# Performance work log

Hardware: AMD Instinct MI355X
Metric: run time of the kernel (lower is better)

Reference implementation:

```python
import jax, jax.numpy as jnp
import numpy as np

B, S, D = 1, 2048, 2048
H = 16
Q_LORA = 1536
KV_LORA = 512
NOPE = 128
ROPE = 64
VD = 128
QHD = NOPE + ROPE  # 192
THETA = 50000.0
EPS = 1e-6


def rmsnorm(x, w, eps=EPS):
    xf = x.astype(jnp.float32)
    var = jnp.mean(xf * xf, axis=-1, keepdims=True)
    return (w * (xf * jax.lax.rsqrt(var + eps)).astype(x.dtype))


def rotate_half(x):
    x1, x2 = jnp.split(x, 2, axis=-1)
    return jnp.concatenate([-x2, x1], axis=-1)


def deinterleave(x):
    # view(..., d//2, 2).transpose(-1,-2).reshape(..., d): [x0,x2,...,x1,x3,...]
    b, h, s, d = x.shape
    return x.reshape(b, h, s, d // 2, 2).swapaxes(-1, -2).reshape(b, h, s, d)


def setup_inputs() -> dict:
    key = jax.random.key(0)
    ks = jax.random.split(key, 8)
    sc = 0.02
    return {
        "hidden_states": jax.random.normal(ks[0], (B, S, D), jnp.float32),
        "position_ids": jnp.broadcast_to(jnp.arange(S, dtype=jnp.int32), (B, S)),
        "q_a_w": jax.random.normal(ks[1], (Q_LORA, D), jnp.float32) * sc,
        "q_a_ln_w": jnp.ones((Q_LORA,), jnp.float32),
        "q_b_w": jax.random.normal(ks[2], (H * QHD, Q_LORA), jnp.float32) * sc,
        "kv_a_w": jax.random.normal(ks[3], (KV_LORA + ROPE, D), jnp.float32) * sc,
        "kv_a_ln_w": jnp.ones((KV_LORA,), jnp.float32),
        "kv_b_w": jax.random.normal(ks[4], (H * (NOPE + VD), KV_LORA), jnp.float32) * sc,
        "o_w": jax.random.normal(ks[5], (D, H * VD), jnp.float32) * sc,
    }


def reference(hidden_states, position_ids, q_a_w, q_a_ln_w, q_b_w, kv_a_w, kv_a_ln_w, kv_b_w, o_w):
    bsz, q_len, _ = hidden_states.shape
    # low-rank Q: q_b(rmsnorm(q_a(x)))
    q = rmsnorm(hidden_states @ q_a_w.T, q_a_ln_w) @ q_b_w.T
    q = q.reshape(bsz, q_len, H, QHD).transpose(0, 2, 1, 3)  # [b,h,s,192]
    q_nope, q_pe = q[..., :NOPE], q[..., NOPE:]
    # compressed KV + shared rope key
    ckv = hidden_states @ kv_a_w.T  # [b,s,512+64]
    compressed_kv, k_pe = ckv[..., :KV_LORA], ckv[..., KV_LORA:]
    k_pe = k_pe.reshape(bsz, q_len, 1, ROPE).transpose(0, 2, 1, 3)  # [b,1,s,64]
    kv = rmsnorm(compressed_kv, kv_a_ln_w) @ kv_b_w.T
    kv = kv.reshape(bsz, q_len, H, NOPE + VD).transpose(0, 2, 1, 3)
    k_nope, value_states = kv[..., :NOPE], kv[..., NOPE:]
    # rotary cache
    inv_freq = 1.0 / (THETA ** (jnp.arange(0, ROPE, 2, dtype=jnp.float32) / ROPE))
    t = jnp.arange(q_len, dtype=jnp.float32)
    freqs = jnp.outer(t, inv_freq)
    emb = jnp.concatenate([freqs, freqs], axis=-1)  # [s,64]
    cos = jnp.cos(emb)[position_ids][:, None]  # [b,1,s,64]
    sin = jnp.sin(emb)[position_ids][:, None]
    q_pe = deinterleave(q_pe)
    k_pe = deinterleave(k_pe)
    q_pe = q_pe * cos + rotate_half(q_pe) * sin
    k_pe = k_pe * cos + rotate_half(k_pe) * sin
    query_states = jnp.concatenate([q_nope, q_pe], axis=-1)  # [b,h,s,192]
    key_states = jnp.concatenate([k_nope, jnp.broadcast_to(k_pe, (bsz, H, q_len, ROPE))], axis=-1)
    scale = QHD ** (-0.5)
    scores = jnp.einsum('bhqd,bhkd->bhqk', query_states, key_states) * scale
    causal = jnp.tril(jnp.ones((q_len, q_len), bool))
    scores = jnp.where(causal, scores, jnp.finfo(scores.dtype).min)
    attn = jax.nn.softmax(scores, axis=-1)
    out = jnp.einsum('bhqk,bhkd->bhqd', attn, value_states)  # [b,h,s,128]
    out = out.transpose(0, 2, 1, 3).reshape(bsz, q_len, H * VD)
    return out @ o_w.T
```

## Files before the change

### kernel.cpp

```cpp
#include <hip/hip_runtime.h>
#include <hip/hip_bf16.h>
#include <cmath>

#define S_LEN 2048
#define D_MODEL 2048
#define N_HEADS 16
#define Q_LORA 1536
#define KV_LORA 512
#define NOPE 128
#define ROPE_D 64
#define VD 128
#define QHD 192
#define AC_W 2112

typedef __attribute__((ext_vector_type(8))) short bf16x8;
typedef __attribute__((ext_vector_type(4))) float f32x4;
typedef __attribute__((ext_vector_type(16))) float f32x16;
typedef __attribute__((ext_vector_type(4))) unsigned short u16x4;

static __device__ __forceinline__ unsigned short f2u(float x) {
  union { float f; unsigned u; } v; v.f = x;
  unsigned r = v.u + 0x7fffu + ((v.u >> 16) & 1u);
  return (unsigned short)(r >> 16);
}
static __device__ __forceinline__ unsigned short f2u_fast(float x) {
  union { float f; unsigned u; } v; v.f = x;
  return (unsigned short)((v.u + 0x8000u) >> 16);
}
static __device__ __forceinline__ float u2f(unsigned short x) {
  union { unsigned u; float f; } v; v.u = ((unsigned)x) << 16;
  return v.f;
}

#define AS1 __attribute__((address_space(1)))
#define AS3 __attribute__((address_space(3)))
static __device__ __forceinline__ void gload_lds16(const unsigned short* g, unsigned short* l) {
  __builtin_amdgcn_global_load_lds((const AS1 unsigned int*)g, (AS3 unsigned int*)l, 16, 0, 0);
}

__global__ __launch_bounds__(256) void conv_bf16(const float* __restrict__ src,
                                                 unsigned short* __restrict__ dst,
                                                 int n4, float scale) {
  for (int i = blockIdx.x * 256 + threadIdx.x; i < n4; i += gridDim.x * 256) {
    const float4 v = ((const float4*)src)[i];
    u16x4 o;
    o[0] = f2u(v.x * scale); o[1] = f2u(v.y * scale);
    o[2] = f2u(v.z * scale); o[3] = f2u(v.w * scale);
    ((u16x4*)dst)[i] = o;
  }
}

__global__ __launch_bounds__(256) void conv2_bf16(const float* __restrict__ srcA, int n4a,
                                                  const float* __restrict__ srcB, int n4total,
                                                  unsigned short* __restrict__ dst) {
  for (int i = blockIdx.x * 256 + threadIdx.x; i < n4total; i += gridDim.x * 256) {
    const float4 v = (i < n4a) ? ((const float4*)srcA)[i] : ((const float4*)srcB)[i - n4a];
    u16x4 o;
    o[0] = f2u(v.x); o[1] = f2u(v.y); o[2] = f2u(v.z); o[3] = f2u(v.w);
    ((u16x4*)dst)[i] = o;
  }
}

template <int MODE>
__global__ __launch_bounds__(256) void gemm_mfma(const unsigned short* __restrict__ A,
                                                 const unsigned short* __restrict__ W,
                                                 void* __restrict__ Cv,
                                                 unsigned short* __restrict__ C2,
                                                 int N, int K) {
  __shared__ unsigned short As[2][8192];
  __shared__ unsigned short Ws[2][4096];
  const int tid = threadIdx.x;
  const int wave = tid >> 6, lane = tid & 63;
  const int col16 = lane & 15, g = lane >> 4;
  const int arow = blockIdx.y * 128, wrow = blockIdx.x * 64;
  const int wm = (wave >> 1) * 64, wn = (wave & 1) * 32;

  const unsigned short* gA[4];
  const unsigned short* gW[2];
  int dA[4], dW[2];
#pragma unroll
  for (int i = 0; i < 4; ++i) {
    const int c = i * 256 + tid;
    const int r = c >> 3, sl = c & 7;
    gA[i] = A + (size_t)(arow + r) * K + (sl ^ (r & 7)) * 8;
    dA[i] = c * 8;
  }
#pragma unroll
  for (int i = 0; i < 2; ++i) {
    const int c = i * 256 + tid;
    const int r = c >> 3, sl = c & 7;
    gW[i] = W + (size_t)(wrow + r) * K + (sl ^ (r & 7)) * 8;
    dW[i] = c * 8;
  }

  f32x4 acc[4][2];
#pragma unroll
  for (int i = 0; i < 4; ++i)
#pragma unroll
    for (int j = 0; j < 2; ++j) acc[i][j] = (f32x4){0.f, 0.f, 0.f, 0.f};

#pragma unroll
  for (int i = 0; i < 4; ++i) gload_lds16(gA[i], &As[0][dA[i]]);
#pragma unroll
  for (int i = 0; i < 2; ++i) gload_lds16(gW[i], &Ws[0][dW[i]]);

  int cur = 0;
  for (int k0 = 0; k0 < K; k0 += 64) {
    __syncthreads();
    if (k0 + 64 < K) {
      const int b = cur ^ 1, kk = k0 + 64;
#pragma unroll
      for (int i = 0; i < 4; ++i) gload_lds16(gA[i] + kk, &As[b][dA[i]]);
#pragma unroll
      for (int i = 0; i < 2; ++i) gload_lds16(gW[i] + kk, &Ws[b][dW[i]]);
    }
#pragma unroll
    for (int kh = 0; kh < 2; ++kh) {
      bf16x8 af[4], bfr[2];
#pragma unroll
      for (int i = 0; i < 4; ++i) {
        const int row = wm + i * 16 + col16;
        af[i] = *(const bf16x8*)(&As[cur][row * 64 + (((kh * 4 + g) ^ (row & 7)) * 8)]);
      }
#pragma unroll
      for (int j = 0; j < 2; ++j) {
        const int row = wn + j * 16 + col16;
        bfr[j] = *(const bf16x8*)(&Ws[cur][row * 64 + (((kh * 4 + g) ^ (row & 7)) * 8)]);
      }
#pragma unroll
      for (int i = 0; i < 4; ++i)
#pragma unroll
        for (int j = 0; j < 2; ++j)
          acc[i][j] = __builtin_amdgcn_mfma_f32_16x16x32_bf16(af[i], bfr[j], acc[i][j], 0, 0, 0);
    }
    cur ^= 1;
  }

#pragma unroll
  for (int i = 0; i < 4; ++i)
#pragma unroll
    for (int j = 0; j < 2; ++j) {
      const int col = wrow + wn + j * 16 + col16;
      const int row0 = arow + wm + i * 16 + g * 4;
#pragma unroll
      for (int r = 0; r < 4; ++r) {
        if constexpr (MODE == 0)
          ((float*)Cv)[(size_t)(row0 + r) * N + col] = acc[i][j][r];
        else if constexpr (MODE == 1)
          ((unsigned short*)Cv)[(size_t)(row0 + r) * N + col] = f2u(acc[i][j][r]);
        else {
          const int hh = col >> 8, d = col & 255;
          if (d < NOPE)
            C2[((size_t)hh * S_LEN + row0 + r) * QHD + d] = f2u(acc[i][j][r]);
          else
            ((unsigned short*)Cv)[(size_t)(row0 + r) * (N_HEADS * 256) + col] = f2u(acc[i][j][r]);
        }
      }
    }
}

__global__ __launch_bounds__(256) void rmsnorm_kernel(const float* __restrict__ src, int src_ld,
                                                      const float* __restrict__ w,
                                                      unsigned short* __restrict__ dst, int dst_ld,
                                                      int dim) {
  const int row = blockIdx.x;
  const float* x = src + (size_t)row * src_ld;
  float ss = 0.f;
  for (int i = threadIdx.x; i < dim; i += 256) {
    float v = x[i];
    ss += v * v;
  }
#pragma unroll
  for (int off = 32; off; off >>= 1) ss += __shfl_xor(ss, off);
  __shared__ float red[4];
  const int wv = threadIdx.x >> 6, ln = threadIdx.x & 63;
  if (ln == 0) red[wv] = ss;
  __syncthreads();
  const float tot = red[0] + red[1] + red[2] + red[3];
  const float scale = rsqrtf(tot / (float)dim + 1e-6f);
  for (int i = threadIdx.x; i < dim; i += 256) {
    dst[(size_t)row * dst_ld + i] = f2u(w[i] * (x[i] * scale));
  }
}

__global__ void rope_kernel(unsigned short* __restrict__ q, const float* __restrict__ ac,
                            unsigned short* __restrict__ Kb, const int* __restrict__ pos_ids) {
  const int s = blockIdx.x;
  const int j = threadIdx.x;
  const float t = (float)pos_ids[s];
  const float invf = powf(50000.0f, -(float)(2 * j) / 64.0f);
  const float ang = t * invf;
  const float c = cosf(ang), sn = sinf(ang);
  for (int h = 0; h < N_HEADS; ++h) {
    unsigned short* base = q + (size_t)s * (N_HEADS * QHD) + h * QHD + NOPE;
    const float x0 = u2f(base[2 * j]), x1 = u2f(base[2 * j + 1]);
    __syncthreads();
    base[j] = f2u(x0 * c - x1 * sn);
    base[32 + j] = f2u(x1 * c + x0 * sn);
    __syncthreads();
  }
  const float* kb = ac + (size_t)s * AC_W + 2048;
  const unsigned short r0 = f2u(kb[2 * j] * c - kb[2 * j + 1] * sn);
  const unsigned short r1 = f2u(kb[2 * j + 1] * c + kb[2 * j] * sn);
#pragma unroll
  for (int h = 0; h < N_HEADS; ++h) {
    unsigned short* kd = Kb + ((size_t)h * S_LEN + s) * QHD + NOPE;
    kd[j] = r0;
    kd[32 + j] = r1;
  }
}

__global__ __launch_bounds__(256) void build_vt(const unsigned short* __restrict__ kv,
                                                unsigned short* __restrict__ Vt) {
  __shared__ unsigned short t[32][33];
  const int s0 = blockIdx.x * 32, d0 = blockIdx.y * 32, h = blockIdx.z;
  const int tx = threadIdx.x & 31, ty = threadIdx.x >> 5;
#pragma unroll
  for (int i = 0; i < 4; ++i) {
    const int s = s0 + ty + i * 8;
    t[ty + i * 8][tx] = kv[(size_t)s * (N_HEADS * 256) + h * 256 + NOPE + d0 + tx];
  }
  __syncthreads();
  const int g16 = tx >> 4, k16 = tx & 15;
  const int h2 = (k16 >> 2) & 1;
  const int jj = (k16 & 3) + 4 * ((k16 >> 3) & 1);
  const int p = g16 * 16 + h2 * 8 + jj;
#pragma unroll
  for (int i = 0; i < 4; ++i) {
    const int d = d0 + ty + i * 8;
    Vt[((size_t)h * VD + d) * S_LEN + s0 + p] = t[tx][ty + i * 8];
  }
}

__global__ __launch_bounds__(256) void flash_attn(const unsigned short* __restrict__ Q,
                                                  const unsigned short* __restrict__ Kb,
                                                  const unsigned short* __restrict__ Vt,
                                                  unsigned short* __restrict__ Pb,
                                                  float2* __restrict__ mlb) {
  __shared__ unsigned short Ks[2][32 * QHD];
  __shared__ unsigned short Vs[2][VD * 32];
  const int tid = threadIdx.x;
  const int wave = tid >> 6, lane = tid & 63;
  const int q5 = lane & 31, h2 = lane >> 5;
  const int lin = (int)blockIdx.x;
  const int h = ((lin & 7) << 1) | ((lin >> 3) & 1);
  const int s = (lin >> 4) & 3;
  const int z = lin >> 6;
  const int za = z >> 2, zb = z & 3;
  const int t = 4 * za + ((za + zb) & 3);
  const int qw = t * 128 + wave * 32;
  const int qr = qw + q5;

  bf16x8 qf[12];
  {
    const unsigned short* qrow = Q + (size_t)qr * (N_HEADS * QHD) + h * QHD + h2 * 8;
#pragma unroll
    for (int i = 0; i < 12; ++i) qf[i] = *(const bf16x8*)(qrow + i * 16);
  }

  const unsigned short* KbH = Kb + (size_t)h * S_LEN * QHD;
  const unsigned short* VtH = Vt + (size_t)h * VD * S_LEN;

  int eK[3], eV[2];
#pragma unroll
  for (int i = 0; i < 3; ++i) {
    const int c = i * 256 + tid;
    const int r = c / 24, sl = c - r * 24;
    eK[i] = r * QHD + (((sl & 24) | ((sl & 7) ^ (r & 7)))) * 8;
  }
#pragma unroll
  for (int i = 0; i < 2; ++i) {
    const int c = i * 256 + tid;
    const int d = c >> 2, sl = c & 3;
    eV[i] = d * S_LEN + ((sl ^ (d & 3))) * 8;
  }

  int xK[12];
#pragma unroll
  for (int i = 0; i < 12; ++i) {
    const int sg = 2 * i + h2;
    xK[i] = q5 * QHD + (((sg & 24) | ((sg & 7) ^ (q5 & 7)))) * 8;
  }
  int xV[2];
#pragma unroll
  for (int i = 0; i < 2; ++i) xV[i] = q5 * 32 + (((i * 2 + h2) ^ (q5 & 3))) * 8;

  f32x16 o[4];
#pragma unroll
  for (int i = 0; i < 4; ++i)
#pragma unroll
    for (int r = 0; r < 16; ++r) o[i][r] = 0.f;
  float m = -1e30f, l = 0.f;

  const int nT = t + 1;

  {
    const unsigned short* kp = KbH + (size_t)s * 32 * QHD;
    const unsigned short* vp = VtH + s * 32;
#pragma unroll
    for (int i = 0; i < 3; ++i) gload_lds16(kp + eK[i], &Ks[0][(i * 256 + tid) * 8]);
#pragma unroll
    for (int i = 0; i < 2; ++i) gload_lds16(vp + eV[i], &Vs[0][(i * 256 + tid) * 8]);
  }

  for (int it = 0; it < nT; ++it) {
    __syncthreads();
    if (it + 1 < nT) {
      const int jn = 4 * (it + 1) + s;
      const unsigned short* kp = KbH + (size_t)jn * 32 * QHD;
      const unsigned short* vp = VtH + jn * 32;
      const int b = (it + 1) & 1;
#pragma unroll
      for (int i = 0; i < 3; ++i) gload_lds16(kp + eK[i], &Ks[b][(i * 256 + tid) * 8]);
#pragma unroll
      for (int i = 0; i < 2; ++i) gload_lds16(vp + eV[i], &Vs[b][(i * 256 + tid) * 8]);
    }
    const int k0 = 32 * (4 * it + s);
    if (k0 <= qw + 31) {
      const unsigned short* Ksc = Ks[it & 1];
      const unsigned short* Vsc = Vs[it & 1];

      f32x16 c;
#pragma unroll
      for (int r = 0; r < 16; ++r) c[r] = 0.f;
      __builtin_amdgcn_s_setprio(1);
#pragma unroll
      for (int dt = 0; dt < 12; ++dt) {
        const bf16x8 a = *(const bf16x8*)(Ksc + xK[dt]);
        c = __builtin_amdgcn_mfma_f32_32x32x16_bf16(a, qf[dt], c, 0, 0, 0);
      }
      __builtin_amdgcn_s_setprio(0);

      if (k0 + 31 > qw) {
#pragma unroll
        for (int r = 0; r < 16; ++r) {
          const int kk = k0 + (r & 3) + 8 * (r >> 2) + 4 * h2;
          if (kk > qr) c[r] = -1e30f;
        }
      }
      float bm = c[0];
#pragma unroll
      for (int r = 1; r < 16; ++r) bm = fmaxf(bm, c[r]);
      bm = fmaxf(bm, __shfl_xor(bm, 32));
      const bool skip = __all(bm <= m + 8.f);
      const float mn = skip ? m : fmaxf(m, bm);
      float ps = 0.f;
      bf16x8 pb0, pb1;
#pragma unroll
      for (int r = 0; r < 8; ++r) {
        const float p0 = exp2f(c[r] - mn);
        const float p1 = exp2f(c[8 + r] - mn);
        ps += p0 + p1;
        pb0[r] = (short)f2u_fast(p0);
        pb1[r] = (short)f2u_fast(p1);
      }
      ps += __shfl_xor(ps, 32);
      if (skip) {
        l += ps;
      } else {
        const float corr = exp2f(m - mn);
        l = l * corr + ps;
        m = mn;
#pragma unroll
        for (int i = 0; i < 4; ++i)
#pragma unroll
          for (int r = 0; r < 16; ++r) o[i][r] *= corr;
      }
      __builtin_amdgcn_s_setprio(1);
#pragma unroll
      for (int db = 0; db < 4; ++db) {
        const bf16x8 va0 = *(const bf16x8*)(Vsc + db * 1024 + xV[0]);
        o[db] = __builtin_amdgcn_mfma_f32_32x32x16_bf16(va0, pb0, o[db], 0, 0, 0);
        const bf16x8 va1 = *(const bf16x8*)(Vsc + db * 1024 + xV[1]);
        o[db] = __builtin_amdgcn_mfma_f32_32x32x16_bf16(va1, pb1, o[db], 0, 0, 0);
      }
      __builtin_amdgcn_s_setprio(0);
    }
  }

  unsigned short* pr = Pb + (((size_t)qr * 4 + s) * N_HEADS + h) * VD;
#pragma unroll
  for (int db = 0; db < 4; ++db)
#pragma unroll
    for (int rq = 0; rq < 4; ++rq) {
      const int d0 = db * 32 + 4 * h2 + 8 * rq;
      u16x4 w4;
      w4[0] = f2u(o[db][rq * 4 + 0]);
      w4[1] = f2u(o[db][rq * 4 + 1]);
      w4[2] = f2u(o[db][rq * 4 + 2]);
      w4[3] = f2u(o[db][rq * 4 + 3]);
      *(uint2*)(pr + d0) = __builtin_bit_cast(uint2, w4);
    }
  if (h2 == 0) mlb[((size_t)qr * 4 + s) * N_HEADS + h] = make_float2(m, l);
}

__global__ __launch_bounds__(256) void combine4(const unsigned short* __restrict__ Pb,
                                                const float2* __restrict__ mlb,
                                                unsigned short* __restrict__ outb) {
  const int idx = blockIdx.x * 256 + threadIdx.x;
  const int d8 = idx & 15, hq = idx >> 4;
  const int h = hq & 15, q = hq >> 4;
  float2 ml[4];
  float M = -1e30f;
#pragma unroll
  for (int s = 0; s < 4; ++s) {
    ml[s] = mlb[((size_t)q * 4 + s) * N_HEADS + h];
    M = fmaxf(M, ml[s].x);
  }
  float w[4], den = 0.f;
#pragma unroll
  for (int s = 0; s < 4; ++s) {
    w[s] = exp2f(ml[s].x - M);
    den += w[s] * ml[s].y;
  }
  const float inv = 1.f / den;
  float acc[8] = {};
#pragma unroll
  for (int s = 0; s < 4; ++s) {
    const bf16x8 v = *(const bf16x8*)(Pb + (((size_t)q * 4 + s) * N_HEADS + h) * VD + d8 * 8);
    const float ws = w[s] * inv;
#pragma unroll
    for (int e = 0; e < 8; ++e) acc[e] += u2f((unsigned short)v[e]) * ws;
  }
  u16x4 o0, o1;
#pragma unroll
  for (int e = 0; e < 4; ++e) { o0[e] = f2u(acc[e]); o1[e] = f2u(acc[4 + e]); }
  unsigned short* dst = outb + ((size_t)q * N_HEADS + h) * VD + d8 * 8;
  *(uint2*)(dst) = __builtin_bit_cast(uint2, o0);
  *(uint2*)(dst + 4) = __builtin_bit_cast(uint2, o1);
}

extern "C" void kernel_launch(void* const* d_in, const int* in_sizes, int n_in,
                              void* d_out, int out_size, void* d_ws, size_t ws_size,
                              hipStream_t stream) {
  const float* hidden    = (const float*)d_in[0];
  const int*   pos       = (const int*)d_in[1];
  const float* q_a_w     = (const float*)d_in[2];
  const float* q_a_ln_w  = (const float*)d_in[3];
  const float* q_b_w     = (const float*)d_in[4];
  const float* kv_a_w    = (const float*)d_in[5];
  const float* kv_a_ln_w = (const float*)d_in[6];
  const float* kv_b_w    = (const float*)d_in[7];
  const float* o_w       = (const float*)d_in[8];
  float* out = (float*)d_out;
  (void)in_sizes; (void)n_in; (void)out_size; (void)ws_size;

  char* base = (char*)d_ws;
  unsigned short* qbuf  = (unsigned short*)(base);
  unsigned short* kvbuf = (unsigned short*)(base + 12582912);
  unsigned short* Pbuf  = (unsigned short*)(base + 12582912);
  float2*         mlb   = (float2*)(base + 46137344);
  float*          ac    = (float*)(base + 29360128);
  unsigned short* qan   = (unsigned short*)(base + 46661632);
  unsigned short* ckvn  = (unsigned short*)(base + 52953088);
  unsigned short* Hb    = (unsigned short*)(base + 55050240);
  unsigned short* Vt    = (unsigned short*)(base + 55050240);
  unsigned short* wbuf  = (unsigned short*)(base + 63438848);
  unsigned short* attnb = (unsigned short*)(base + 72876032);
  unsigned short* Kb    = (unsigned short*)(base + 81264640);

  const dim3 b256(256);
  const float qscale = 0.07216878364870323f * 1.4426950408889634f;

  conv_bf16<<<2048, b256, 0, stream>>>(hidden, Hb, (S_LEN * D_MODEL) / 4, 1.f);

  conv2_bf16<<<2048, b256, 0, stream>>>(q_a_w, (Q_LORA * D_MODEL) / 4,
                                        kv_a_w, (AC_W * D_MODEL) / 4, wbuf);
  gemm_mfma<0><<<dim3(AC_W / 64, S_LEN / 128), b256, 0, stream>>>(Hb, wbuf, ac, nullptr, AC_W, D_MODEL);

  rmsnorm_kernel<<<S_LEN, b256, 0, stream>>>(ac, AC_W, q_a_ln_w, qan, Q_LORA, Q_LORA);
  rmsnorm_kernel<<<S_LEN, b256, 0, stream>>>(ac + Q_LORA, AC_W, kv_a_ln_w, ckvn, KV_LORA, KV_LORA);

  conv_bf16<<<2048, b256, 0, stream>>>(q_b_w, wbuf, (N_HEADS * QHD * Q_LORA) / 4, qscale);
  gemm_mfma<1><<<dim3(N_HEADS * QHD / 64, S_LEN / 128), b256, 0, stream>>>(qan, wbuf, qbuf, nullptr, N_HEADS * QHD, Q_LORA);

  conv_bf16<<<2048, b256, 0, stream>>>(kv_b_w, wbuf, (N_HEADS * 256 * KV_LORA) / 4, 1.f);
  gemm_mfma<2><<<dim3(N_HEADS * 256 / 64, S_LEN / 128), b256, 0, stream>>>(ckvn, wbuf, kvbuf, Kb, N_HEADS * 256, KV_LORA);

  rope_kernel<<<S_LEN, 32, 0, stream>>>(qbuf, ac, Kb, pos);

  build_vt<<<dim3(S_LEN / 32, VD / 32, N_HEADS), b256, 0, stream>>>(kvbuf, Vt);

  flash_attn<<<dim3(1024), b256, 0, stream>>>(qbuf, Kb, Vt, Pbuf, mlb);
  combine4<<<2048, b256, 0, stream>>>(Pbuf, mlb, attnb);

  conv_bf16<<<2048, b256, 0, stream>>>(o_w, wbuf, (D_MODEL * N_HEADS * VD) / 4, 1.f);
  gemm_mfma<0><<<dim3(D_MODEL / 64, S_LEN / 128), b256, 0, stream>>>(attnb, wbuf, out, nullptr, D_MODEL, N_HEADS * VD);
}
```

Before: 213.4 us.

## Switch flash attention from 32x32x16 to 16x16x32 MFMA tiles

Each wave now handles its 32 query rows as two 16-row halves and uses 16x16x32 bf16 MFMA instructions for both QK^T and PV. The K and V shared-memory read swizzles are redone to match, and build_vt's permutation of V columns is changed so its layout fits the new B-operand layout. The aim is better MFMA throughput or issue efficiency and a softmax that works on smaller accumulator tiles. The cost is twice the softmax bookkeeping (two running max/sum states), extra cross-lane shuffles, and more MFMA instructions per tile.

```diff
diff --git a/kernel.cpp b/kernel.cpp
--- a/kernel.cpp
+++ b/kernel.cpp
@@ -15,7 +15,6 @@
 
 typedef __attribute__((ext_vector_type(8))) short bf16x8;
 typedef __attribute__((ext_vector_type(4))) float f32x4;
-typedef __attribute__((ext_vector_type(16))) float f32x16;
 typedef __attribute__((ext_vector_type(4))) unsigned short u16x4;
 
 static __device__ __forceinline__ unsigned short f2u(float x) {
@@ -221,10 +220,7 @@
     t[ty + i * 8][tx] = kv[(size_t)s * (N_HEADS * 256) + h * 256 + NOPE + d0 + tx];
   }
   __syncthreads();
-  const int g16 = tx >> 4, k16 = tx & 15;
-  const int h2 = (k16 >> 2) & 1;
-  const int jj = (k16 & 3) + 4 * ((k16 >> 3) & 1);
-  const int p = g16 * 16 + h2 * 8 + jj;
+  const int p = ((tx & 15) >> 2) * 8 + ((tx >> 4) & 1) * 4 + (tx & 3);
 #pragma unroll
   for (int i = 0; i < 4; ++i) {
     const int d = d0 + ty + i * 8;
@@ -241,21 +237,25 @@
   __shared__ unsigned short Vs[2][VD * 32];
   const int tid = threadIdx.x;
   const int wave = tid >> 6, lane = tid & 63;
-  const int q5 = lane & 31, h2 = lane >> 5;
+  const int g = lane >> 4, col = lane & 15;
   const int lin = (int)blockIdx.x;
   const int h = ((lin & 7) << 1) | ((lin >> 3) & 1);
   const int s = (lin >> 4) & 3;
   const int z = lin >> 6;
-  const int za = z >> 2, zb = z & 3;
-  const int t = 4 * za + ((za + zb) & 3);
-  const int qw = t * 128 + wave * 32;
-  const int qr = qw + q5;
-
-  bf16x8 qf[12];
+  const int zj = z >> 2, za = z & 3;
+  const int t = 4 * zj + ((zj + za) & 3);
+  const int qwv = t * 128 + wave * 32;
+  const int qrA = qwv + col, qrB = qwv + 16 + col;
+
+  bf16x8 qfA[6], qfB[6];
   {
-    const unsigned short* qrow = Q + (size_t)qr * (N_HEADS * QHD) + h * QHD + h2 * 8;
-#pragma unroll
-    for (int i = 0; i < 12; ++i) qf[i] = *(const bf16x8*)(qrow + i * 16);
+    const unsigned short* qa = Q + (size_t)qrA * (N_HEADS * QHD) + h * QHD + g * 8;
+    const unsigned short* qb = Q + (size_t)qrB * (N_HEADS * QHD) + h * QHD + g * 8;
+#pragma unroll
+    for (int i = 0; i < 6; ++i) {
+      qfA[i] = *(const bf16x8*)(qa + i * 32);
+      qfB[i] = *(const bf16x8*)(qb + i * 32);
+    }
   }
 
   const unsigned short* KbH = Kb + (size_t)h * S_LEN * QHD;
@@ -275,22 +275,13 @@
     eV[i] = d * S_LEN + ((sl ^ (d & 3))) * 8;
   }
 
-  int xK[12];
-#pragma unroll
-  for (int i = 0; i < 12; ++i) {
-    const int sg = 2 * i + h2;
-    xK[i] = q5 * QHD + (((sg & 24) | ((sg & 7) ^ (q5 & 7)))) * 8;
-  }
-  int xV[2];
-#pragma unroll
-  for (int i = 0; i < 2; ++i) xV[i] = q5 * 32 + (((i * 2 + h2) ^ (q5 & 3))) * 8;
-
-  f32x16 o[4];
-#pragma unroll
-  for (int i = 0; i < 4; ++i)
-#pragma unroll
-    for (int r = 0; r < 16; ++r) o[i][r] = 0.f;
-  float m = -1e30f, l = 0.f;
+  f32x4 oA[8], oB[8];
+#pragma unroll
+  for (int i = 0; i < 8; ++i) {
+    oA[i] = (f32x4){0.f, 0.f, 0.f, 0.f};
+    oB[i] = (f32x4){0.f, 0.f, 0.f, 0.f};
+  }
+  float mA = -1e30f, lA = 0.f, mB = -1e30f, lB = 0.f;
 
   const int nT = t + 1;
 
@@ -302,6 +293,13 @@
 #pragma unroll
     for (int i = 0; i < 2; ++i) gload_lds16(vp + eV[i], &Vs[0][(i * 256 + tid) * 8]);
   }
+
+  int xK[6];
+#pragma unroll
+  for (int i = 0; i < 6; ++i) xK[i] = ((4 * i + g) ^ (col & 7)) * 8;
+  const int rbK = col * QHD;
+  const int xV = (g ^ (col & 3)) * 8;
+  const int rbV = col * 32;
 
   for (int it = 0; it < nT; ++it) {
     __syncthreads();
@@ -316,82 +314,122 @@
       for (int i = 0; i < 2; ++i) gload_lds16(vp + eV[i], &Vs[b][(i * 256 + tid) * 8]);
     }
     const int k0 = 32 * (4 * it + s);
-    if (k0 <= qw + 31) {
+    if (k0 <= qwv + 31) {
       const unsigned short* Ksc = Ks[it & 1];
       const unsigned short* Vsc = Vs[it & 1];
 
-      f32x16 c;
-#pragma unroll
-      for (int r = 0; r < 16; ++r) c[r] = 0.f;
+      f32x4 cA0 = (f32x4){0.f, 0.f, 0.f, 0.f}, cA1 = cA0, cB0 = cA0, cB1 = cA0;
       __builtin_amdgcn_s_setprio(1);
 #pragma unroll
-      for (int dt = 0; dt < 12; ++dt) {
-        const bf16x8 a = *(const bf16x8*)(Ksc + xK[dt]);
-        c = __builtin_amdgcn_mfma_f32_32x32x16_bf16(a, qf[dt], c, 0, 0, 0);
+      for (int dt = 0; dt < 6; ++dt) {
+        const bf16x8 a0 = *(const bf16x8*)(Ksc + rbK + xK[dt]);
+        const bf16x8 a1 = *(const bf16x8*)(Ksc + rbK + 16 * QHD + xK[dt]);
+        cA0 = __builtin_amdgcn_mfma_f32_16x16x32_bf16(a0, qfA[dt], cA0, 0, 0, 0);
+        cA1 = __builtin_amdgcn_mfma_f32_16x16x32_bf16(a1, qfA[dt], cA1, 0, 0, 0);
+        cB0 = __builtin_amdgcn_mfma_f32_16x16x32_bf16(a0, qfB[dt], cB0, 0, 0, 0);
+        cB1 = __builtin_amdgcn_mfma_f32_16x16x32_bf16(a1, qfB[dt], cB1, 0, 0, 0);
       }
       __builtin_amdgcn_s_setprio(0);
 
-      if (k0 + 31 > qw) {
-#pragma unroll
-        for (int r = 0; r < 16; ++r) {
-          const int kk = k0 + (r & 3) + 8 * (r >> 2) + 4 * h2;
-          if (kk > qr) c[r] = -1e30f;
+      if (k0 + 31 > qwv) {
+#pragma unroll
+        for (int r = 0; r < 4; ++r) {
+          const int kk = k0 + 4 * g + r;
+          if (kk > qrA) cA0[r] = -1e30f;
+          if (kk + 16 > qrA) cA1[r] = -1e30f;
+          if (kk > qrB) cB0[r] = -1e30f;
+          if (kk + 16 > qrB) cB1[r] = -1e30f;
         }
       }
-      float bm = c[0];
-#pragma unroll
-      for (int r = 1; r < 16; ++r) bm = fmaxf(bm, c[r]);
-      bm = fmaxf(bm, __shfl_xor(bm, 32));
-      const bool skip = __all(bm <= m + 8.f);
-      const float mn = skip ? m : fmaxf(m, bm);
-      float ps = 0.f;
-      bf16x8 pb0, pb1;
-#pragma unroll
-      for (int r = 0; r < 8; ++r) {
-        const float p0 = exp2f(c[r] - mn);
-        const float p1 = exp2f(c[8 + r] - mn);
-        ps += p0 + p1;
-        pb0[r] = (short)f2u_fast(p0);
-        pb1[r] = (short)f2u_fast(p1);
-      }
-      ps += __shfl_xor(ps, 32);
-      if (skip) {
-        l += ps;
-      } else {
-        const float corr = exp2f(m - mn);
-        l = l * corr + ps;
-        m = mn;
-#pragma unroll
-        for (int i = 0; i < 4; ++i)
-#pragma unroll
-          for (int r = 0; r < 16; ++r) o[i][r] *= corr;
+      bf16x8 pbA, pbB;
+      {
+        float bm = fmaxf(fmaxf(fmaxf(cA0[0], cA0[1]), fmaxf(cA0[2], cA0[3])),
+                         fmaxf(fmaxf(cA1[0], cA1[1]), fmaxf(cA1[2], cA1[3])));
+        bm = fmaxf(bm, __shfl_xor(bm, 16));
+        bm = fmaxf(bm, __shfl_xor(bm, 32));
+        const bool skip = __all(bm <= mA + 8.f);
+        const float mn = skip ? mA : fmaxf(mA, bm);
+        float ps = 0.f;
+#pragma unroll
+        for (int r = 0; r < 4; ++r) {
+          const float p0 = exp2f(cA0[r] - mn);
+          const float p1 = exp2f(cA1[r] - mn);
+          ps += p0 + p1;
+          pbA[r] = (short)f2u_fast(p0);
+          pbA[4 + r] = (short)f2u_fast(p1);
+        }
+        ps += __shfl_xor(ps, 16);
+        ps += __shfl_xor(ps, 32);
+        if (skip) {
+          lA += ps;
+        } else {
+          const float corr = exp2f(mA - mn);
+          lA = lA * corr + ps;
+          mA = mn;
+#pragma unroll
+          for (int i = 0; i < 8; ++i) {
+            oA[i][0] *= corr; oA[i][1] *= corr; oA[i][2] *= corr; oA[i][3] *= corr;
+          }
+        }
+      }
+      {
+        float bm = fmaxf(fmaxf(fmaxf(cB0[0], cB0[1]), fmaxf(cB0[2], cB0[3])),
+                         fmaxf(fmaxf(cB1[0], cB1[1]), fmaxf(cB1[2], cB1[3])));
+        bm = fmaxf(bm, __shfl_xor(bm, 16));
+        bm = fmaxf(bm, __shfl_xor(bm, 32));
+        const bool skip = __all(bm <= mB + 8.f);
+        const float mn = skip ? mB : fmaxf(mB, bm);
+        float ps = 0.f;
+#pragma unroll
+        for (int r = 0; r < 4; ++r) {
+          const float p0 = exp2f(cB0[r] - mn);
+          const float p1 = exp2f(cB1[r] - mn);
+          ps += p0 + p1;
+          pbB[r] = (short)f2u_fast(p0);
+          pbB[4 + r] = (short)f2u_fast(p1);
+        }
+        ps += __shfl_xor(ps, 16);
+        ps += __shfl_xor(ps, 32);
+        if (skip) {
+          lB += ps;
+        } else {
+          const float corr = exp2f(mB - mn);
+          lB = lB * corr + ps;
+          mB = mn;
+#pragma unroll
+          for (int i = 0; i < 8; ++i) {
+            oB[i][0] *= corr; oB[i][1] *= corr; oB[i][2] *= corr; oB[i][3] *= corr;
+          }
+        }
       }
       __builtin_amdgcn_s_setprio(1);
 #pragma unroll
-      for (int db = 0; db < 4; ++db) {
-        const bf16x8 va0 = *(const bf16x8*)(Vsc + db * 1024 + xV[0]);
-        o[db] = __builtin_amdgcn_mfma_f32_32x32x16_bf16(va0, pb0, o[db], 0, 0, 0);
-        const bf16x8 va1 = *(const bf16x8*)(Vsc + db * 1024 + xV[1]);
-        o[db] = __builtin_amdgcn_mfma_f32_32x32x16_bf16(va1, pb1, o[db], 0, 0, 0);
+      for (int db = 0; db < 8; ++db) {
+        const bf16x8 va = *(const bf16x8*)(Vsc + db * 512 + rbV + xV);
+        oA[db] = __builtin_amdgcn_mfma_f32_16x16x32_bf16(va, pbA, oA[db], 0, 0, 0);
+        oB[db] = __builtin_amdgcn_mfma_f32_16x16x32_bf16(va, pbB, oB[db], 0, 0, 0);
       }
       __builtin_amdgcn_s_setprio(0);
     }
   }
 
-  unsigned short* pr = Pb + (((size_t)qr * 4 + s) * N_HEADS + h) * VD;
-#pragma unroll
-  for (int db = 0; db < 4; ++db)
-#pragma unroll
-    for (int rq = 0; rq < 4; ++rq) {
-      const int d0 = db * 32 + 4 * h2 + 8 * rq;
-      u16x4 w4;
-      w4[0] = f2u(o[db][rq * 4 + 0]);
-      w4[1] = f2u(o[db][rq * 4 + 1]);
-      w4[2] = f2u(o[db][rq * 4 + 2]);
-      w4[3] = f2u(o[db][rq * 4 + 3]);
-      *(uint2*)(pr + d0) = __builtin_bit_cast(uint2, w4);
-    }
-  if (h2 == 0) mlb[((size_t)qr * 4 + s) * N_HEADS + h] = make_float2(m, l);
+  unsigned short* prA = Pb + (((size_t)qrA * 4 + s) * N_HEADS + h) * VD;
+  unsigned short* prB = Pb + (((size_t)qrB * 4 + s) * N_HEADS + h) * VD;
+#pragma unroll
+  for (int db = 0; db < 8; ++db) {
+    u16x4 wa, wb;
+#pragma unroll
+    for (int r = 0; r < 4; ++r) {
+      wa[r] = f2u(oA[db][r]);
+      wb[r] = f2u(oB[db][r]);
+    }
+    *(uint2*)(prA + db * 16 + 4 * g) = __builtin_bit_cast(uint2, wa);
+    *(uint2*)(prB + db * 16 + 4 * g) = __builtin_bit_cast(uint2, wb);
+  }
+  if (g == 0) {
+    mlb[((size_t)qrA * 4 + s) * N_HEADS + h] = make_float2(mA, lA);
+    mlb[((size_t)qrB * 4 + s) * N_HEADS + h] = make_float2(mB, lB);
+  }
 }
 
 __global__ __launch_bounds__(256) void combine4(const unsigned short* __restrict__ Pb,
```

Measured after the change: 219.2 us. +2.7%, slower.
